# Performance work log

Hardware: AMD Instinct MI355X
Metric: run time of the kernel (lower is better)

## Reference

```python
import jax, jax.numpy as jnp
import numpy as np

HID = 16
DATA_DIM = 2
B = 2048
T = 64
RTOL, ATOL = 1e-2, 1e-4
SAFETY, FMIN, FMAX = 0.9, 0.2, 10.0
MAX_STEPS = 16  # bounded adaptive-step budget (masked once t reaches T1)
T1 = 1.0
DT0 = 1.0

# Tsit5 (Tsitouras 2011) tableau
_A2 = (0.161,)
_A3 = (-0.008480655492356989, 0.335480655492357)
_A4 = (2.8971530571054935, -6.359448489975075, 4.3622954328695815)
_A5 = (5.325864828439257, -11.748883564062828, 7.4955393428898365, -0.09249506636175525)
_A6 = (5.86145544294642, -12.92096931784711, 8.159367898576159, -0.071584973281401, -0.028269050394068383)
_B5 = (0.09646076681806523, 0.01, 0.4798896504144996, 1.379008574103742, -3.290069515436081, 2.324710524099774)
_BT = (-0.00178001105222577714, -0.0008164344596567469, 0.007880878010261995, -0.1447110071732629, 0.5823571654525552, -0.45808210592918697, 0.015151515151515152)


def setup_inputs() -> dict:
    key = jax.random.key(0)
    ks = jax.random.split(key, 13)
    u = lambda k, shape, fan: jax.random.uniform(k, shape, jnp.float32, -1.0, 1.0) / np.float32(np.sqrt(fan))
    return dict(
        x_seq=jax.random.normal(ks[0], (B, T, DATA_DIM), jnp.float32),
        w1=u(ks[1], (HID, HID), HID), b1=u(ks[2], (HID,), HID),
        w2=u(ks[3], (HID, HID), HID), b2=u(ks[4], (HID,), HID),
        w3=u(ks[5], (HID, HID), HID), b3=u(ks[6], (HID,), HID),
        gru_wih=u(ks[7], (3 * HID, DATA_DIM), DATA_DIM),
        gru_whh=u(ks[8], (3 * HID, HID), HID),
        gru_b=u(ks[9], (3 * HID,), HID),
        gru_bn=u(ks[10], (HID,), HID),
        pred_w=u(ks[11], (1, HID), HID),
        pred_b=u(ks[12], (1,), HID),
    )


def _mlp(y, w1, b1, w2, b2, w3, b3):
    # eqx.nn.MLP(in=16, out=16, width=16, depth=2, activation=tanh): 3 Linear layers
    y = jnp.tanh(y @ w1.T + b1)
    y = jnp.tanh(y @ w2.T + b2)
    return y @ w3.T + b3


def _ode_solve(h0, f):
    """Adaptive Tsit5 + I-controller (diffrax PIDController defaults) from t=0 to t=1.
    Per-sample adaptive step/accept/reject, batched over the leading axis."""
    nB = h0.shape[0]

    def body(state, _):
        y, t, dt = state                      # y:[B,16]  t,dt:[B]
        dt_c = jnp.minimum(dt, T1 - t)        # clip so we never overshoot t1
        d = dt_c[:, None]
        k1 = f(y)
        k2 = f(y + d * (_A2[0] * k1))
        k3 = f(y + d * (_A3[0] * k1 + _A3[1] * k2))
        k4 = f(y + d * (_A4[0] * k1 + _A4[1] * k2 + _A4[2] * k3))
        k5 = f(y + d * (_A5[0] * k1 + _A5[1] * k2 + _A5[2] * k3 + _A5[3] * k4))
        k6 = f(y + d * (_A6[0] * k1 + _A6[1] * k2 + _A6[2] * k3 + _A6[3] * k4 + _A6[4] * k5))
        y_new = y + d * (_B5[0] * k1 + _B5[1] * k2 + _B5[2] * k3 + _B5[3] * k4 + _B5[4] * k5 + _B5[5] * k6)
        k7 = f(y_new)                          # FSAL stage, enters only the error estimate
        err = d * (_BT[0] * k1 + _BT[1] * k2 + _BT[2] * k3 + _BT[3] * k4 + _BT[4] * k5 + _BT[5] * k6 + _BT[6] * k7)
        scale = ATOL + RTOL * jnp.maximum(jnp.abs(y), jnp.abs(y_new))
        err2 = jnp.maximum(jnp.mean((err / scale) ** 2, axis=-1), 1e-16)  # squared RMS norm, [B]
        accept = err2 <= 1.0
        y = jnp.where(accept[:, None], y_new, y)
        t = jnp.where(accept, t + dt_c, t)
        # I-controller: factor = safety * err_norm**(-1/order), order=5
        factor = jnp.clip(SAFETY * err2 ** (-0.1), FMIN, FMAX)
        dt = dt_c * factor
        return (y, t, dt), None

    init = (h0, jnp.zeros((nB,), h0.dtype), jnp.full((nB,), DT0, h0.dtype))
    (y, _, _), _ = jax.lax.scan(body, init, None, length=MAX_STEPS)
    return y


def _gru(x, h, wih, whh, b, bn):
    # eqx.nn.GRUCell math
    ig = x @ wih.T + b
    hg = h @ whh.T
    ir, iz, inn = jnp.split(ig, 3, axis=-1)
    hr, hz, hn = jnp.split(hg, 3, axis=-1)
    r = jax.nn.sigmoid(ir + hr)
    z = jax.nn.sigmoid(iz + hz)
    n = jnp.tanh(inn + r * (hn + bn))
    return n + z * (h - n)


def reference(x_seq, w1, b1, w2, b2, w3, b3, gru_wih, gru_whh, gru_b, gru_bn, pred_w, pred_b):
    f = lambda y: _mlp(y, w1, b1, w2, b2, w3, b3)
    h0 = jnp.zeros((x_seq.shape[0], HID), x_seq.dtype)

    def step(h, x_t):
        h_ev = _ode_solve(h, f)
        h_new = _gru(x_t, h_ev, gru_wih, gru_whh, gru_b, gru_bn)
        return h_new, None

    xs = jnp.swapaxes(x_seq, 0, 1)  # [T, B, D]
    h_final, _ = jax.lax.scan(step, h0, xs)
    return h_final @ pred_w.T + pred_b  # [B, 1]
```

## Files before the change

kernel.cpp:

```cpp
#include <hip/hip_runtime.h>


#define T_STEPS 64
#define NB 2048
#define N_ODE_STEPS 16

typedef float v2f __attribute__((ext_vector_type(2)));

__device__ __forceinline__ v2f make2(float a, float b) { v2f r; r.x = a; r.y = b; return r; }

#define ROR(x, r) __int_as_float(__builtin_amdgcn_update_dpp( \
    0, __float_as_int(x), 0x120 + (r), 0xF, 0xF, true))

__device__ __forceinline__ float rsum16(float v) {
  v += ROR(v, 8);
  v += ROR(v, 4);
  v += ROR(v, 2);
  v += ROR(v, 1);
  return v;
}

__constant__ int O_[16] = {0,8,4,12,2,10,6,14,1,9,5,13,3,11,7,15};

__device__ __forceinline__ void gather16(float y, v2f (&G)[8]) {
  float g0 = y;
  float g1 = ROR(g0, 8);
  float g2 = ROR(g0, 4);
  float g3 = ROR(g1, 4);
  float g4 = ROR(g0, 2);
  float g5 = ROR(g1, 2);
  float g6 = ROR(g2, 2);
  float g7 = ROR(g3, 2);
  float g8  = ROR(g0, 1);
  float g9  = ROR(g1, 1);
  float g10 = ROR(g2, 1);
  float g11 = ROR(g3, 1);
  float g12 = ROR(g4, 1);
  float g13 = ROR(g5, 1);
  float g14 = ROR(g6, 1);
  float g15 = ROR(g7, 1);
  G[0] = make2(g0,  g1);  G[1] = make2(g2,  g3);
  G[2] = make2(g4,  g5);  G[3] = make2(g6,  g7);
  G[4] = make2(g8,  g9);  G[5] = make2(g10, g11);
  G[6] = make2(g12, g13); G[7] = make2(g14, g15);
}

__device__ __forceinline__ float dot8pk(const v2f (&W)[8], const v2f (&G)[8], float bias) {
  v2f a0 = __builtin_elementwise_fma(G[0], W[0], make2(bias, 0.0f));
  v2f a1 = G[1] * W[1];
  a0 = __builtin_elementwise_fma(G[2], W[2], a0);
  a1 = __builtin_elementwise_fma(G[3], W[3], a1);
  a0 = __builtin_elementwise_fma(G[4], W[4], a0);
  a1 = __builtin_elementwise_fma(G[5], W[5], a1);
  a0 = __builtin_elementwise_fma(G[6], W[6], a0);
  a1 = __builtin_elementwise_fma(G[7], W[7], a1);
  v2f s = a0 + a1;
  return s.x + s.y;
}

__device__ __forceinline__ float fast_tanh(float x) {
  float e = __builtin_amdgcn_exp2f(x * 2.885390081777927f);
  return fmaf(-2.0f, __builtin_amdgcn_rcpf(e + 1.0f), 1.0f);
}

__device__ __forceinline__ float sigmoid_(float x) {
  float e = __builtin_amdgcn_exp2f(x * -1.4426950408889634f);
  return __builtin_amdgcn_rcpf(1.0f + e);
}

__device__ __forceinline__ float mlp_f(float y,
    const v2f (&w1p)[8], float b1v,
    const v2f (&w2p)[8], float b2v,
    const v2f (&w3p)[8], float b3v) {
  v2f G[8];
  gather16(y, G);
  float h1 = fast_tanh(dot8pk(w1p, G, b1v));
  gather16(h1, G);
  float h2 = fast_tanh(dot8pk(w2p, G, b2v));
  gather16(h2, G);
  return dot8pk(w3p, G, b3v);
}

__global__
__attribute__((amdgpu_flat_work_group_size(64, 64), amdgpu_waves_per_eu(1, 1)))
void odern_kernel(
    const float* __restrict__ x_seq,
    const float* __restrict__ w1, const float* __restrict__ b1,
    const float* __restrict__ w2, const float* __restrict__ b2,
    const float* __restrict__ w3, const float* __restrict__ b3,
    const float* __restrict__ gru_wih, const float* __restrict__ gru_whh,
    const float* __restrict__ gru_b, const float* __restrict__ gru_bn,
    const float* __restrict__ pred_w, const float* __restrict__ pred_b,
    float* __restrict__ out) {
  const int tid = threadIdx.x;
  const int j = tid & 15;
  const int g = tid >> 4;
  const int b = blockIdx.x * 4 + g;

  v2f w1p[8], w2p[8], w3p[8], whp[8], wzp[8], wnp[8];
#pragma unroll
  for (int p = 0; p < 8; ++p) {
    const int ia = (j - O_[2 * p]) & 15;
    const int ib = (j - O_[2 * p + 1]) & 15;
    w1p[p] = make2(w1[j * 16 + ia], w1[j * 16 + ib]);
    w2p[p] = make2(w2[j * 16 + ia], w2[j * 16 + ib]);
    w3p[p] = make2(w3[j * 16 + ia], w3[j * 16 + ib]);
    whp[p] = make2(gru_whh[j * 16 + ia],        gru_whh[j * 16 + ib]);
    wzp[p] = make2(gru_whh[(16 + j) * 16 + ia], gru_whh[(16 + j) * 16 + ib]);
    wnp[p] = make2(gru_whh[(32 + j) * 16 + ia], gru_whh[(32 + j) * 16 + ib]);
  }
  const float b1v = b1[j], b2v = b2[j], b3v = b3[j];
  const float wih_r0 = gru_wih[j * 2],        wih_r1 = gru_wih[j * 2 + 1];
  const float wih_z0 = gru_wih[(16 + j) * 2], wih_z1 = gru_wih[(16 + j) * 2 + 1];
  const float wih_n0 = gru_wih[(32 + j) * 2], wih_n1 = gru_wih[(32 + j) * 2 + 1];
  const float gb_r = gru_b[j], gb_z = gru_b[16 + j], gb_n = gru_b[32 + j];
  const float bnv = gru_bn[j];
  const float pwv = pred_w[j], pbv = pred_b[0];

  const float* xp = x_seq + (size_t)b * (T_STEPS * 2);

  float h = 0.0f;
#pragma unroll 1
  for (int t = 0; t < T_STEPS; ++t) {
    const float x0 = xp[2 * t];
    const float x1 = xp[2 * t + 1];

    float y = h;
    float tt = 0.0f, dt = 1.0f;
    float k1 = mlp_f(y, w1p, b1v, w2p, b2v, w3p, b3v);
#pragma unroll 1
    for (int s = 0; s < N_ODE_STEPS; ++s) {
      if (__all(tt >= 1.0f)) break;

      const float dt_c = fminf(dt, 1.0f - tt);
      const float d = dt_c;

      float s2 = 0.161f * k1;
      float k2 = mlp_f(fmaf(d, s2, y), w1p, b1v, w2p, b2v, w3p, b3v);

      float s3 = fmaf(0.335480655492357f, k2, -0.008480655492356989f * k1);
      float k3 = mlp_f(fmaf(d, s3, y), w1p, b1v, w2p, b2v, w3p, b3v);

      float s4 = fmaf(4.3622954328695815f, k3,
                 fmaf(-6.359448489975075f, k2, 2.8971530571054935f * k1));
      float k4 = mlp_f(fmaf(d, s4, y), w1p, b1v, w2p, b2v, w3p, b3v);

      float s5 = fmaf(-0.09249506636175525f, k4,
                 fmaf(7.4955393428898365f, k3,
                 fmaf(-11.748883564062828f, k2, 5.325864828439257f * k1)));
      float k5 = mlp_f(fmaf(d, s5, y), w1p, b1v, w2p, b2v, w3p, b3v);

      float s6 = fmaf(-0.028269050394068383f, k5,
                 fmaf(-0.071584973281401f, k4,
                 fmaf(8.159367898576159f, k3,
                 fmaf(-12.92096931784711f, k2, 5.86145544294642f * k1))));
      float k6 = mlp_f(fmaf(d, s6, y), w1p, b1v, w2p, b2v, w3p, b3v);

      float sy = fmaf(2.324710524099774f, k6,
                 fmaf(-3.290069515436081f, k5,
                 fmaf(1.379008574103742f, k4,
                 fmaf(0.4798896504144996f, k3,
                 fmaf(0.01f, k2, 0.09646076681806523f * k1)))));
      float y_new = fmaf(d, sy, y);

      float k7 = mlp_f(y_new, w1p, b1v, w2p, b2v, w3p, b3v);

      float se = fmaf(0.015151515151515152f, k7,
                 fmaf(-0.45808210592918697f, k6,
                 fmaf(0.5823571654525552f, k5,
                 fmaf(-0.1447110071732629f, k4,
                 fmaf(0.007880878010261995f, k3,
                 fmaf(-0.0008164344596567469f, k2, -0.001780011052225777f * k1))))));
      float err = d * se;

      float scale = fmaf(0.01f, fmaxf(fabsf(y), fabsf(y_new)), 0.0001f);
      float r = err * __builtin_amdgcn_rcpf(scale);
      float m = rsum16(r * r) * 0.0625f;
      float err2 = fmaxf(m, 1e-16f);

      const bool acc = err2 <= 1.0f;
      y = acc ? y_new : y;
      tt = acc ? tt + dt_c : tt;
      k1 = acc ? k7 : k1;

      float fac = 0.9f * __builtin_amdgcn_exp2f(-0.1f * __builtin_amdgcn_logf(err2));
      fac = fminf(fmaxf(fac, 0.2f), 10.0f);
      dt = dt_c * fac;
    }

    float ir = fmaf(wih_r1, x1, fmaf(wih_r0, x0, gb_r));
    float iz = fmaf(wih_z1, x1, fmaf(wih_z0, x0, gb_z));
    float in_ = fmaf(wih_n1, x1, fmaf(wih_n0, x0, gb_n));
    v2f G[8];
    gather16(y, G);
    float pre_r = dot8pk(whp, G, ir);
    float pre_z = dot8pk(wzp, G, iz);
    float hnb   = dot8pk(wnp, G, bnv);
    float rg = sigmoid_(pre_r);
    float zg = sigmoid_(pre_z);
    float ng = fast_tanh(fmaf(rg, hnb, in_));
    h = fmaf(zg, y - ng, ng);
  }

  float ps = rsum16(h * pwv);
  if (j == 0) out[b] = ps + pbv;
}

extern "C" void kernel_launch(void* const* d_in, const int* in_sizes, int n_in,
                              void* d_out, int out_size, void* d_ws, size_t ws_size,
                              hipStream_t stream) {
  (void)in_sizes; (void)n_in; (void)out_size; (void)d_ws; (void)ws_size;
  odern_kernel<<<dim3(NB / 4), dim3(64), 0, stream>>>(
      (const float*)d_in[0],
      (const float*)d_in[1], (const float*)d_in[2],
      (const float*)d_in[3], (const float*)d_in[4],
      (const float*)d_in[5], (const float*)d_in[6],
      (const float*)d_in[7], (const float*)d_in[8],
      (const float*)d_in[9], (const float*)d_in[10],
      (const float*)d_in[11], (const float*)d_in[12],
      (float*)d_out);
}
```

Measured before the change: 188.5 us.

## Simplify DPP gather, force packed FMA asm, rebalance Tsit5 sums, move exit check

Several changes at once. The 16-lane gather now uses direct row-rotates by 1..15 instead of a dependent tree of rotates, which shortens the dependency chain at the cost of reordering the weight permutation. Packed FMAs are emitted through inline asm. The Tsit5 stage combinations are split into parallel partial sums to cut serial FMA latency. The waves-per-EU cap is removed and the early-exit vote moves to the end of each step. The reassociated sums slightly change rounding.

```diff
diff --git a/kernel.cpp b/kernel.cpp
--- a/kernel.cpp
+++ b/kernel.cpp
@@ -11,6 +11,12 @@
 
 #define ROR(x, r) __int_as_float(__builtin_amdgcn_update_dpp( \
     0, __float_as_int(x), 0x120 + (r), 0xF, 0xF, true))
+
+__device__ __forceinline__ v2f pkfma(v2f a, v2f b, v2f c) {
+  v2f d;
+  asm("v_pk_fma_f32 %0, %1, %2, %3" : "=v"(d) : "v"(a), "v"(b), "v"(c));
+  return d;
+}
 
 __device__ __forceinline__ float rsum16(float v) {
   v += ROR(v, 8);
@@ -20,40 +26,26 @@
   return v;
 }
 
-__constant__ int O_[16] = {0,8,4,12,2,10,6,14,1,9,5,13,3,11,7,15};
-
 __device__ __forceinline__ void gather16(float y, v2f (&G)[8]) {
-  float g0 = y;
-  float g1 = ROR(g0, 8);
-  float g2 = ROR(g0, 4);
-  float g3 = ROR(g1, 4);
-  float g4 = ROR(g0, 2);
-  float g5 = ROR(g1, 2);
-  float g6 = ROR(g2, 2);
-  float g7 = ROR(g3, 2);
-  float g8  = ROR(g0, 1);
-  float g9  = ROR(g1, 1);
-  float g10 = ROR(g2, 1);
-  float g11 = ROR(g3, 1);
-  float g12 = ROR(g4, 1);
-  float g13 = ROR(g5, 1);
-  float g14 = ROR(g6, 1);
-  float g15 = ROR(g7, 1);
-  G[0] = make2(g0,  g1);  G[1] = make2(g2,  g3);
-  G[2] = make2(g4,  g5);  G[3] = make2(g6,  g7);
-  G[4] = make2(g8,  g9);  G[5] = make2(g10, g11);
-  G[6] = make2(g12, g13); G[7] = make2(g14, g15);
+  G[0] = make2(y,          ROR(y, 1));
+  G[1] = make2(ROR(y, 2),  ROR(y, 3));
+  G[2] = make2(ROR(y, 4),  ROR(y, 5));
+  G[3] = make2(ROR(y, 6),  ROR(y, 7));
+  G[4] = make2(ROR(y, 8),  ROR(y, 9));
+  G[5] = make2(ROR(y, 10), ROR(y, 11));
+  G[6] = make2(ROR(y, 12), ROR(y, 13));
+  G[7] = make2(ROR(y, 14), ROR(y, 15));
 }
 
 __device__ __forceinline__ float dot8pk(const v2f (&W)[8], const v2f (&G)[8], float bias) {
-  v2f a0 = __builtin_elementwise_fma(G[0], W[0], make2(bias, 0.0f));
+  v2f a0 = pkfma(G[0], W[0], make2(bias, 0.0f));
   v2f a1 = G[1] * W[1];
-  a0 = __builtin_elementwise_fma(G[2], W[2], a0);
-  a1 = __builtin_elementwise_fma(G[3], W[3], a1);
-  a0 = __builtin_elementwise_fma(G[4], W[4], a0);
-  a1 = __builtin_elementwise_fma(G[5], W[5], a1);
-  a0 = __builtin_elementwise_fma(G[6], W[6], a0);
-  a1 = __builtin_elementwise_fma(G[7], W[7], a1);
+  a0 = pkfma(G[2], W[2], a0);
+  a1 = pkfma(G[3], W[3], a1);
+  a0 = pkfma(G[4], W[4], a0);
+  a1 = pkfma(G[5], W[5], a1);
+  a0 = pkfma(G[6], W[6], a0);
+  a1 = pkfma(G[7], W[7], a1);
   v2f s = a0 + a1;
   return s.x + s.y;
 }
@@ -82,7 +74,7 @@
 }
 
 __global__
-__attribute__((amdgpu_flat_work_group_size(64, 64), amdgpu_waves_per_eu(1, 1)))
+__attribute__((amdgpu_flat_work_group_size(64, 64)))
 void odern_kernel(
     const float* __restrict__ x_seq,
     const float* __restrict__ w1, const float* __restrict__ b1,
@@ -100,8 +92,8 @@
   v2f w1p[8], w2p[8], w3p[8], whp[8], wzp[8], wnp[8];
 #pragma unroll
   for (int p = 0; p < 8; ++p) {
-    const int ia = (j - O_[2 * p]) & 15;
-    const int ib = (j - O_[2 * p + 1]) & 15;
+    const int ia = (j - 2 * p) & 15;
+    const int ib = (j - 2 * p - 1) & 15;
     w1p[p] = make2(w1[j * 16 + ia], w1[j * 16 + ib]);
     w2p[p] = make2(w2[j * 16 + ia], w2[j * 16 + ib]);
     w3p[p] = make2(w3[j * 16 + ia], w3[j * 16 + ib]);
@@ -130,47 +122,41 @@
     float k1 = mlp_f(y, w1p, b1v, w2p, b2v, w3p, b3v);
 #pragma unroll 1
     for (int s = 0; s < N_ODE_STEPS; ++s) {
-      if (__all(tt >= 1.0f)) break;
-
       const float dt_c = fminf(dt, 1.0f - tt);
       const float d = dt_c;
 
       float s2 = 0.161f * k1;
       float k2 = mlp_f(fmaf(d, s2, y), w1p, b1v, w2p, b2v, w3p, b3v);
 
-      float s3 = fmaf(0.335480655492357f, k2, -0.008480655492356989f * k1);
+      float s3 = fmaf(-0.008480655492356989f, k1, 0.335480655492357f * k2);
       float k3 = mlp_f(fmaf(d, s3, y), w1p, b1v, w2p, b2v, w3p, b3v);
 
-      float s4 = fmaf(4.3622954328695815f, k3,
-                 fmaf(-6.359448489975075f, k2, 2.8971530571054935f * k1));
+      float u4 = fmaf(-6.359448489975075f, k2, 2.8971530571054935f * k1);
+      float s4 = fmaf(4.3622954328695815f, k3, u4);
       float k4 = mlp_f(fmaf(d, s4, y), w1p, b1v, w2p, b2v, w3p, b3v);
 
-      float s5 = fmaf(-0.09249506636175525f, k4,
-                 fmaf(7.4955393428898365f, k3,
-                 fmaf(-11.748883564062828f, k2, 5.325864828439257f * k1)));
+      float u5a = fmaf(-11.748883564062828f, k2, 5.325864828439257f * k1);
+      float u5b = fmaf(-0.09249506636175525f, k4, 7.4955393428898365f * k3);
+      float s5 = u5a + u5b;
       float k5 = mlp_f(fmaf(d, s5, y), w1p, b1v, w2p, b2v, w3p, b3v);
 
-      float s6 = fmaf(-0.028269050394068383f, k5,
-                 fmaf(-0.071584973281401f, k4,
-                 fmaf(8.159367898576159f, k3,
-                 fmaf(-12.92096931784711f, k2, 5.86145544294642f * k1))));
+      float u6a = fmaf(-12.92096931784711f, k2, 5.86145544294642f * k1);
+      float u6b = fmaf(-0.071584973281401f, k4, 8.159367898576159f * k3);
+      float s6 = fmaf(-0.028269050394068383f, k5, u6a + u6b);
       float k6 = mlp_f(fmaf(d, s6, y), w1p, b1v, w2p, b2v, w3p, b3v);
 
-      float sy = fmaf(2.324710524099774f, k6,
-                 fmaf(-3.290069515436081f, k5,
-                 fmaf(1.379008574103742f, k4,
-                 fmaf(0.4798896504144996f, k3,
-                 fmaf(0.01f, k2, 0.09646076681806523f * k1)))));
+      float uya = fmaf(0.01f, k2, 0.09646076681806523f * k1);
+      float uyb = fmaf(1.379008574103742f, k4, 0.4798896504144996f * k3);
+      float uyc = fmaf(2.324710524099774f, k6, -3.290069515436081f * k5);
+      float sy = (uya + uyb) + uyc;
       float y_new = fmaf(d, sy, y);
 
       float k7 = mlp_f(y_new, w1p, b1v, w2p, b2v, w3p, b3v);
 
-      float se = fmaf(0.015151515151515152f, k7,
-                 fmaf(-0.45808210592918697f, k6,
-                 fmaf(0.5823571654525552f, k5,
-                 fmaf(-0.1447110071732629f, k4,
-                 fmaf(0.007880878010261995f, k3,
-                 fmaf(-0.0008164344596567469f, k2, -0.001780011052225777f * k1))))));
+      float uea = fmaf(-0.0008164344596567469f, k2, -0.001780011052225777f * k1);
+      float ueb = fmaf(-0.1447110071732629f, k4, 0.007880878010261995f * k3);
+      float uec = fmaf(-0.45808210592918697f, k6, 0.5823571654525552f * k5);
+      float se = (uea + ueb) + fmaf(0.015151515151515152f, k7, uec);
       float err = d * se;
 
       float scale = fmaf(0.01f, fmaxf(fabsf(y), fabsf(y_new)), 0.0001f);
@@ -182,6 +168,8 @@
       y = acc ? y_new : y;
       tt = acc ? tt + dt_c : tt;
       k1 = acc ? k7 : k1;
+
+      if (__all(tt >= 1.0f)) break;
 
       float fac = 0.9f * __builtin_amdgcn_exp2f(-0.1f * __builtin_amdgcn_logf(err2));
       fac = fminf(fmaxf(fac, 0.2f), 10.0f);
```

After: 191.8 us. No clear change (+1.8%).
